# Performance work log

Measured on AMD Instinct MI355X. Metric: run time of the kernel, lower is better.

## Reference

```python
import jax, jax.numpy as jnp
from jax import lax
import numpy as np


def setup_inputs() -> dict:
    key = jax.random.key(0)
    kx, = jax.random.split(key, 1)
    B, T = 4096, 4096
    x = jax.random.normal(kx, (B, T), dtype=jnp.float32)
    omega_log = jnp.asarray(0.0, dtype=jnp.float32)
    alpha_log = jnp.asarray(0.0, dtype=jnp.float32)
    beta_log = jnp.asarray(0.0, dtype=jnp.float32)
    return {"x": x, "omega_log": omega_log, "alpha_log": alpha_log, "beta_log": beta_log}


def reference(x, omega_log, alpha_log, beta_log):
    # x: [B, T]
    ea = jnp.exp(alpha_log)
    eb = jnp.exp(beta_log)
    denom = 1.0 + ea + eb
    omega = jnp.exp(omega_log)
    alpha = ea / denom
    beta = eb / denom

    # initial variance: unbiased sample variance over time (torch.var default ddof=1)
    s0 = jnp.var(x, axis=1, ddof=1)  # [B]

    xsq = jnp.swapaxes(x[:, :-1] ** 2, 0, 1)  # [T-1, B]

    def step(s_prev, x2_t):
        s_t = omega + alpha * x2_t + beta * s_prev
        return s_t, s_t

    _, rest = lax.scan(step, s0, xsq)  # rest: [T-1, B]
    sigma2 = jnp.concatenate([s0[None, :], rest], axis=0)  # [T, B]
    return jnp.sqrt(jnp.swapaxes(sigma2, 0, 1))  # [B, T]
```

## Files before the change

kernel.cpp:

```cpp
#include <hip/hip_runtime.h>
#include <math.h>

#define B_ROWS 4096
#define T_COLS 4096
#define NTHREADS 256
#define CHUNK 16
#define NWAVES (NTHREADS / 64)
#define CSTRIDE 20

__device__ __forceinline__ float rfl(float v) {
    return __int_as_float(__builtin_amdgcn_readfirstlane(__float_as_int(v)));
}

__global__ __launch_bounds__(NTHREADS) void garch_fused(
    const float* __restrict__ x,
    const float* __restrict__ p_omega_log,
    const float* __restrict__ p_alpha_log,
    const float* __restrict__ p_beta_log,
    float* __restrict__ out)
{
    __shared__ float lds[NTHREADS * CSTRIDE];
    __shared__ float wA[NWAVES], wB[NWAVES], rSum[NWAVES], rSsq[NWAVES];

    const int t    = threadIdx.x;
    const int lane = t & 63;
    const int wv   = t >> 6;
    const long rbase = (long)blockIdx.x * T_COLS;

    float ea_p = expf(p_alpha_log[0]);
    float eb_p = expf(p_beta_log[0]);
    float denom = 1.0f + ea_p + eb_p;
    float omega = rfl(expf(p_omega_log[0]));
    float alpha = rfl(ea_p / denom);
    float beta  = rfl(eb_p / denom);

    float bpow[CHUNK + 1];
    bpow[0] = 1.0f;
#pragma unroll
    for (int j = 1; j <= CHUNK; ++j) bpow[j] = bpow[j - 1] * beta;

    const float4* xv = reinterpret_cast<const float4*>(x + rbase);
#pragma unroll
    for (int k = 0; k < 4; ++k) {
        int f = k * 256 + t;
        float4 v = xv[f];
        int c = f >> 2, j = f & 3;
        *reinterpret_cast<float4*>(&lds[c * CSTRIDE + j * 4]) = v;
    }
    __syncthreads();

    float xr[CHUNK];
#pragma unroll
    for (int j = 0; j < 4; ++j) {
        float4 v = *reinterpret_cast<const float4*>(&lds[t * CSTRIDE + j * 4]);
        xr[4 * j + 0] = v.x; xr[4 * j + 1] = v.y;
        xr[4 * j + 2] = v.z; xr[4 * j + 3] = v.w;
    }
    float prev = (t > 0) ? lds[(t - 1) * CSTRIDE + 15] : 0.0f;

    float sum = 0.0f, ssq = 0.0f;
#pragma unroll
    for (int i = 0; i < CHUNK; ++i) { sum += xr[i]; ssq = fmaf(xr[i], xr[i], ssq); }

    float Z[CHUNK];
    float z;
    if (t > 0) { z = fmaf(alpha, prev * prev, omega); Z[0] = z; }
    else       { z = 0.0f;                            Z[0] = 0.0f; }
#pragma unroll
    for (int i = 0; i < CHUNK - 1; ++i) {
        z = fmaf(beta, z, fmaf(alpha, xr[i] * xr[i], omega));
        Z[i + 1] = z;
    }
    float bpart = z;
    float apart = (t == 0) ? bpow[15] : bpow[16];

    float s1 = sum, s2 = ssq;
#pragma unroll
    for (int d = 32; d > 0; d >>= 1) {
        s1 += __shfl_xor(s1, d);
        s2 += __shfl_xor(s2, d);
    }

    float ia = apart, ib = bpart;
#pragma unroll
    for (int d = 1; d < 64; d <<= 1) {
        float pa = __shfl_up(ia, d);
        float pb = __shfl_up(ib, d);
        if (lane >= d) { ib = fmaf(ia, pb, ib); ia = ia * pa; }
    }

    if (lane == 0)  { rSum[wv] = s1; rSsq[wv] = s2; }
    if (lane == 63) { wA[wv] = ia;   wB[wv] = ib;  }
    __syncthreads();

    float tsum = rSum[0] + rSum[1] + rSum[2] + rSum[3];
    float tssq = rSsq[0] + rSsq[1] + rSsq[2] + rSsq[3];
    float s0 = (tssq - tsum * tsum * (1.0f / T_COLS)) * (1.0f / (T_COLS - 1));
    s0 = fmaxf(s0, 0.0f);

    float sw = s0;
#pragma unroll
    for (int w = 0; w < NWAVES - 1; ++w)
        if (w < wv) sw = fmaf(wA[w], sw, wB[w]);

    float pea = __shfl_up(ia, 1);
    float peb = __shfl_up(ib, 1);
    if (lane == 0) { pea = 1.0f; peb = 0.0f; }
    float s = fmaf(pea, sw, peb);

    if (t == 0) {
        float4 q0;
        q0.x = __builtin_amdgcn_sqrtf(s);
        q0.y = __builtin_amdgcn_sqrtf(fmaf(bpow[1], s, Z[1]));
        q0.z = __builtin_amdgcn_sqrtf(fmaf(bpow[2], s, Z[2]));
        q0.w = __builtin_amdgcn_sqrtf(fmaf(bpow[3], s, Z[3]));
        *reinterpret_cast<float4*>(&lds[t * CSTRIDE]) = q0;
#pragma unroll
        for (int k = 1; k < 4; ++k) {
            float4 q;
            q.x = __builtin_amdgcn_sqrtf(fmaf(bpow[4 * k + 0], s, Z[4 * k + 0]));
            q.y = __builtin_amdgcn_sqrtf(fmaf(bpow[4 * k + 1], s, Z[4 * k + 1]));
            q.z = __builtin_amdgcn_sqrtf(fmaf(bpow[4 * k + 2], s, Z[4 * k + 2]));
            q.w = __builtin_amdgcn_sqrtf(fmaf(bpow[4 * k + 3], s, Z[4 * k + 3]));
            *reinterpret_cast<float4*>(&lds[t * CSTRIDE + 4 * k]) = q;
        }
    } else {
#pragma unroll
        for (int k = 0; k < 4; ++k) {
            float4 q;
            q.x = __builtin_amdgcn_sqrtf(fmaf(bpow[4 * k + 1], s, Z[4 * k + 0]));
            q.y = __builtin_amdgcn_sqrtf(fmaf(bpow[4 * k + 2], s, Z[4 * k + 1]));
            q.z = __builtin_amdgcn_sqrtf(fmaf(bpow[4 * k + 3], s, Z[4 * k + 2]));
            q.w = __builtin_amdgcn_sqrtf(fmaf(bpow[4 * k + 4], s, Z[4 * k + 3]));
            *reinterpret_cast<float4*>(&lds[t * CSTRIDE + 4 * k]) = q;
        }
    }
    __syncthreads();

    float4* ov = reinterpret_cast<float4*>(out + rbase);
#pragma unroll
    for (int k = 0; k < 4; ++k) {
        int f = k * 256 + t;
        int c = f >> 2, j = f & 3;
        ov[f] = *reinterpret_cast<const float4*>(&lds[c * CSTRIDE + j * 4]);
    }
}

extern "C" void kernel_launch(void* const* d_in, const int* in_sizes, int n_in,
                              void* d_out, int out_size, void* d_ws, size_t ws_size,
                              hipStream_t stream) {
    const float* x         = (const float*)d_in[0];
    const float* omega_log = (const float*)d_in[1];
    const float* alpha_log = (const float*)d_in[2];
    const float* beta_log  = (const float*)d_in[3];
    float* out = (float*)d_out;

    garch_fused<<<B_ROWS, NTHREADS, 0, stream>>>(x, omega_log, alpha_log, beta_log, out);
}
```

Baseline: 114.0 us.

## Use 1024 threads with 4 contiguous elements each and drop the LDS transpose

The block grows to 1024 threads, each owning one float4 of the row, so global loads and stores are coalesced directly and the LDS staging buffer, its transposes and one barrier go away. The neighbouring element comes from a wave shuffle, with a global load at wave boundaries. Outputs are recomputed by running the recurrence forward from the carried-in state, which replaces the stored Z array and beta powers. The cross-wave combine now runs serially over 16 waves instead of 4, and the scan tree covers more elements.

Measured after the change: 127.1 us. 1.11x slower.

```diff
diff --git a/kernel.cpp b/kernel.cpp
--- a/kernel.cpp
+++ b/kernel.cpp
@@ -3,23 +3,21 @@
 
 #define B_ROWS 4096
 #define T_COLS 4096
-#define NTHREADS 256
-#define CHUNK 16
+#define NTHREADS 1024
+#define CHUNK 4
 #define NWAVES (NTHREADS / 64)
-#define CSTRIDE 20
 
 __device__ __forceinline__ float rfl(float v) {
     return __int_as_float(__builtin_amdgcn_readfirstlane(__float_as_int(v)));
 }
 
-__global__ __launch_bounds__(NTHREADS) void garch_fused(
+__global__ __launch_bounds__(NTHREADS, 8) void garch_fused(
     const float* __restrict__ x,
     const float* __restrict__ p_omega_log,
     const float* __restrict__ p_alpha_log,
     const float* __restrict__ p_beta_log,
     float* __restrict__ out)
 {
-    __shared__ float lds[NTHREADS * CSTRIDE];
     __shared__ float wA[NWAVES], wB[NWAVES], rSum[NWAVES], rSsq[NWAVES];
 
     const int t    = threadIdx.x;
@@ -27,52 +25,38 @@
     const int wv   = t >> 6;
     const long rbase = (long)blockIdx.x * T_COLS;
 
-    float ea_p = expf(p_alpha_log[0]);
-    float eb_p = expf(p_beta_log[0]);
+    float4 v = reinterpret_cast<const float4*>(x + rbase)[t];
+
+    float prevg = 0.0f;
+    if (lane == 0 && t > 0) prevg = x[rbase + 4 * t - 1];
+
+    float ea_p  = expf(p_alpha_log[0]);
+    float eb_p  = expf(p_beta_log[0]);
     float denom = 1.0f + ea_p + eb_p;
     float omega = rfl(expf(p_omega_log[0]));
     float alpha = rfl(ea_p / denom);
     float beta  = rfl(eb_p / denom);
+    float beta2 = beta * beta;
+    float beta3 = beta2 * beta;
+    float beta4 = beta2 * beta2;
 
-    float bpow[CHUNK + 1];
-    bpow[0] = 1.0f;
-#pragma unroll
-    for (int j = 1; j <= CHUNK; ++j) bpow[j] = bpow[j - 1] * beta;
+    float x0 = v.x, x1 = v.y, x2 = v.z, x3 = v.w;
 
-    const float4* xv = reinterpret_cast<const float4*>(x + rbase);
-#pragma unroll
-    for (int k = 0; k < 4; ++k) {
-        int f = k * 256 + t;
-        float4 v = xv[f];
-        int c = f >> 2, j = f & 3;
-        *reinterpret_cast<float4*>(&lds[c * CSTRIDE + j * 4]) = v;
-    }
-    __syncthreads();
+    float prev = __shfl_up(x3, 1);
+    if (lane == 0) prev = prevg;
 
-    float xr[CHUNK];
-#pragma unroll
-    for (int j = 0; j < 4; ++j) {
-        float4 v = *reinterpret_cast<const float4*>(&lds[t * CSTRIDE + j * 4]);
-        xr[4 * j + 0] = v.x; xr[4 * j + 1] = v.y;
-        xr[4 * j + 2] = v.z; xr[4 * j + 3] = v.w;
-    }
-    float prev = (t > 0) ? lds[(t - 1) * CSTRIDE + 15] : 0.0f;
+    float sum = ((x0 + x1) + (x2 + x3));
+    float ssq = x0 * x0;
+    ssq = fmaf(x1, x1, ssq);
+    ssq = fmaf(x2, x2, ssq);
+    ssq = fmaf(x3, x3, ssq);
 
-    float sum = 0.0f, ssq = 0.0f;
-#pragma unroll
-    for (int i = 0; i < CHUNK; ++i) { sum += xr[i]; ssq = fmaf(xr[i], xr[i], ssq); }
-
-    float Z[CHUNK];
-    float z;
-    if (t > 0) { z = fmaf(alpha, prev * prev, omega); Z[0] = z; }
-    else       { z = 0.0f;                            Z[0] = 0.0f; }
-#pragma unroll
-    for (int i = 0; i < CHUNK - 1; ++i) {
-        z = fmaf(beta, z, fmaf(alpha, xr[i] * xr[i], omega));
-        Z[i + 1] = z;
-    }
+    float z = (t > 0) ? fmaf(alpha, prev * prev, omega) : 0.0f;
+    z = fmaf(beta, z, fmaf(alpha, x0 * x0, omega));
+    z = fmaf(beta, z, fmaf(alpha, x1 * x1, omega));
+    z = fmaf(beta, z, fmaf(alpha, x2 * x2, omega));
     float bpart = z;
-    float apart = (t == 0) ? bpow[15] : bpow[16];
+    float apart = (t == 0) ? beta3 : beta4;
 
     float s1 = sum, s2 = ssq;
 #pragma unroll
@@ -93,8 +77,9 @@
     if (lane == 63) { wA[wv] = ia;   wB[wv] = ib;  }
     __syncthreads();
 
-    float tsum = rSum[0] + rSum[1] + rSum[2] + rSum[3];
-    float tssq = rSsq[0] + rSsq[1] + rSsq[2] + rSsq[3];
+    float tsum = 0.0f, tssq = 0.0f;
+#pragma unroll
+    for (int w = 0; w < NWAVES; ++w) { tsum += rSum[w]; tssq += rSsq[w]; }
     float s0 = (tssq - tsum * tsum * (1.0f / T_COLS)) * (1.0f / (T_COLS - 1));
     s0 = fmaxf(s0, 0.0f);
 
@@ -108,42 +93,22 @@
     if (lane == 0) { pea = 1.0f; peb = 0.0f; }
     float s = fmaf(pea, sw, peb);
 
+    float4 q;
     if (t == 0) {
-        float4 q0;
-        q0.x = __builtin_amdgcn_sqrtf(s);
-        q0.y = __builtin_amdgcn_sqrtf(fmaf(bpow[1], s, Z[1]));
-        q0.z = __builtin_amdgcn_sqrtf(fmaf(bpow[2], s, Z[2]));
-        q0.w = __builtin_amdgcn_sqrtf(fmaf(bpow[3], s, Z[3]));
-        *reinterpret_cast<float4*>(&lds[t * CSTRIDE]) = q0;
-#pragma unroll
-        for (int k = 1; k < 4; ++k) {
-            float4 q;
-            q.x = __builtin_amdgcn_sqrtf(fmaf(bpow[4 * k + 0], s, Z[4 * k + 0]));
-            q.y = __builtin_amdgcn_sqrtf(fmaf(bpow[4 * k + 1], s, Z[4 * k + 1]));
-            q.z = __builtin_amdgcn_sqrtf(fmaf(bpow[4 * k + 2], s, Z[4 * k + 2]));
-            q.w = __builtin_amdgcn_sqrtf(fmaf(bpow[4 * k + 3], s, Z[4 * k + 3]));
-            *reinterpret_cast<float4*>(&lds[t * CSTRIDE + 4 * k]) = q;
-        }
+        q.x = __builtin_amdgcn_sqrtf(s);
+        float zz = s;
+        zz = fmaf(beta, zz, fmaf(alpha, x0 * x0, omega)); q.y = __builtin_amdgcn_sqrtf(zz);
+        zz = fmaf(beta, zz, fmaf(alpha, x1 * x1, omega)); q.z = __builtin_amdgcn_sqrtf(zz);
+        zz = fmaf(beta, zz, fmaf(alpha, x2 * x2, omega)); q.w = __builtin_amdgcn_sqrtf(zz);
     } else {
-#pragma unroll
-        for (int k = 0; k < 4; ++k) {
-            float4 q;
-            q.x = __builtin_amdgcn_sqrtf(fmaf(bpow[4 * k + 1], s, Z[4 * k + 0]));
-            q.y = __builtin_amdgcn_sqrtf(fmaf(bpow[4 * k + 2], s, Z[4 * k + 1]));
-            q.z = __builtin_amdgcn_sqrtf(fmaf(bpow[4 * k + 3], s, Z[4 * k + 2]));
-            q.w = __builtin_amdgcn_sqrtf(fmaf(bpow[4 * k + 4], s, Z[4 * k + 3]));
-            *reinterpret_cast<float4*>(&lds[t * CSTRIDE + 4 * k]) = q;
-        }
+        float zz = s;
+        zz = fmaf(beta, zz, fmaf(alpha, prev * prev, omega)); q.x = __builtin_amdgcn_sqrtf(zz);
+        zz = fmaf(beta, zz, fmaf(alpha, x0 * x0, omega));     q.y = __builtin_amdgcn_sqrtf(zz);
+        zz = fmaf(beta, zz, fmaf(alpha, x1 * x1, omega));     q.z = __builtin_amdgcn_sqrtf(zz);
+        zz = fmaf(beta, zz, fmaf(alpha, x2 * x2, omega));     q.w = __builtin_amdgcn_sqrtf(zz);
     }
-    __syncthreads();
 
-    float4* ov = reinterpret_cast<float4*>(out + rbase);
-#pragma unroll
-    for (int k = 0; k < 4; ++k) {
-        int f = k * 256 + t;
-        int c = f >> 2, j = f & 3;
-        ov[f] = *reinterpret_cast<const float4*>(&lds[c * CSTRIDE + j * 4]);
-    }
+    reinterpret_cast<float4*>(out + rbase)[t] = q;
 }
 
 extern "C" void kernel_launch(void* const* d_in, const int* in_sizes, int n_in,
```
